# Performance work log

Hardware: AMD Instinct MI355X
Metric: run time of the kernel (lower is better)

The kernel has to match this reference:

```python
import jax, jax.numpy as jnp
import numpy as np

N_PROJECT = 100000
N_COMPANY = 50000
N_EDGES = 1000000
INPUT_DIM = 256
HIDDEN_DIM = 128
NUM_LAYERS = 2
EPS = 1e-12


def setup_inputs() -> dict:
    key = jax.random.key(0)
    ks = jax.random.split(key, 10)
    return {
        "x_project": jax.random.normal(ks[0], (N_PROJECT, INPUT_DIM), jnp.float32),
        "x_company": jax.random.normal(ks[1], (N_COMPANY, INPUT_DIM), jnp.float32),
        "W_project": jax.random.normal(ks[2], (INPUT_DIM, HIDDEN_DIM), jnp.float32) * 0.05,
        "b_project": jax.random.normal(ks[3], (HIDDEN_DIM,), jnp.float32) * 0.05,
        "W_company": jax.random.normal(ks[4], (INPUT_DIM, HIDDEN_DIM), jnp.float32) * 0.05,
        "b_company": jax.random.normal(ks[5], (HIDDEN_DIM,), jnp.float32) * 0.05,
        "pc_src": jax.random.randint(ks[6], (N_EDGES,), 0, N_PROJECT, jnp.int32),
        "pc_dst": jax.random.randint(ks[7], (N_EDGES,), 0, N_COMPANY, jnp.int32),
        "cp_src": jax.random.randint(ks[8], (N_EDGES,), 0, N_COMPANY, jnp.int32),
        "cp_dst": jax.random.randint(ks[9], (N_EDGES,), 0, N_PROJECT, jnp.int32),
    }


def _rel_aggregate(x_src, row, col, num_src, num_dst):
    # D_src^-1/2 A D_dst^-1/2 normalized gather-scale-scatter_add for one relation.
    ones = jnp.ones(row.shape[0], jnp.float32)
    deg_s = jax.ops.segment_sum(ones, row, num_segments=num_src)
    deg_d = jax.ops.segment_sum(ones, col, num_segments=num_dst)
    inv_s = jnp.where(deg_s > 0, deg_s ** -0.5, 0.0)
    inv_d = jnp.where(deg_d > 0, deg_d ** -0.5, 0.0)
    w = inv_s[row] * inv_d[col]                      # [E]
    msg = x_src[row] * w[:, None]                    # [E, H]
    return jax.ops.segment_sum(msg, col, num_segments=num_dst)  # [num_dst, H]


def reference(x_project, x_company, W_project, b_project, W_company, b_company,
              pc_src, pc_dst, cp_src, cp_dst):
    h_p = x_project @ W_project + b_project          # [Np, H]
    h_c = x_company @ W_company + b_company          # [Nc, H]
    acc_p, acc_c = h_p, h_c
    for _ in range(NUM_LAYERS):
        new_p = _rel_aggregate(h_c, cp_src, cp_dst, N_COMPANY, N_PROJECT)
        new_c = _rel_aggregate(h_p, pc_src, pc_dst, N_PROJECT, N_COMPANY)
        h_p, h_c = new_p, new_c
        acc_p = acc_p + h_p
        acc_c = acc_c + h_c
    scale = 1.0 / (NUM_LAYERS + 1)
    out_p = acc_p * scale
    out_c = acc_c * scale
    # F.normalize(p=2, dim=-1)
    out_p = out_p / jnp.maximum(jnp.linalg.norm(out_p, axis=-1, keepdims=True), EPS)
    out_c = out_c / jnp.maximum(jnp.linalg.norm(out_c, axis=-1, keepdims=True), EPS)
    return out_p, out_c
```

## Files before the change

kernel.cpp:

```cpp
#include <hip/hip_runtime.h>
#include <hip/hip_bf16.h>
#include <math.h>

#define HD 128
#define KD 256
#define CAP 64
#define CAPA 96
#define BA 128

typedef __attribute__((ext_vector_type(8))) short bf16x8;
typedef __attribute__((ext_vector_type(4))) float f32x4;

__device__ __forceinline__ unsigned short bfbits(float x) {
    __hip_bfloat16 h = __float2bfloat16(x);
    return *(unsigned short*)&h;
}
__device__ __forceinline__ unsigned int pack_bf2(float a, float b) {
    __hip_bfloat162 h;
    h.x = __float2bfloat16(a);
    h.y = __float2bfloat16(b);
    return *(unsigned int*)&h;
}
__device__ __forceinline__ float2 unpack_bf2(unsigned int u) {
    __hip_bfloat162 h = *(__hip_bfloat162*)&u;
    return __bfloat1622float2(h);
}
__device__ __forceinline__ bf16x8 cvt8(float4 a, float4 b) {
    bf16x8 r;
    r[0] = (short)bfbits(a.x); r[1] = (short)bfbits(a.y);
    r[2] = (short)bfbits(a.z); r[3] = (short)bfbits(a.w);
    r[4] = (short)bfbits(b.x); r[5] = (short)bfbits(b.y);
    r[6] = (short)bfbits(b.z); r[7] = (short)bfbits(b.w);
    return r;
}

__launch_bounds__(256)
__global__ void phaseA(
        const int* __restrict__ cps, const int* __restrict__ cpd,
        int* __restrict__ db0, int* __restrict__ sb0, int* cntD0, int* cntS0,
        const int* __restrict__ pcs, const int* __restrict__ pcd,
        int* __restrict__ db1, int* __restrict__ sb1, int* cntD1, int* cntS1,
        int E, int G0, int G1,
        const float* __restrict__ WA, unsigned short* __restrict__ WtA,
        const float* __restrict__ WB, unsigned short* __restrict__ WtB) {
    __shared__ int curD[512], curS[512];
    const int b = blockIdx.x;
    if (b >= 2 * BA) {
        int idx = (b - 2 * BA) * 256 + threadIdx.x;
        const float* W = (idx < KD * HD) ? WA : WB;
        unsigned short* Wt = (idx < KD * HD) ? WtA : WtB;
        int id = idx & (KD * HD - 1);
        int j = id & 7, lane = (id >> 3) & 63, nt = (id >> 9) & 7, kc = id >> 12;
        int k = kc * 32 + (lane >> 4) * 8 + j;
        int c = nt * 16 + (lane & 15);
        Wt[id] = bfbits(W[k * HD + c]);
        return;
    }
    const int rel = b >> 7;
    const int ib  = b & (BA - 1);
    const int* src = rel ? pcs : cps;
    const int* dst = rel ? pcd : cpd;
    int* db   = rel ? db1 : db0;
    int* sb   = rel ? sb1 : sb0;
    int* cntD = rel ? cntD1 : cntD0;
    int* cntS = rel ? cntS1 : cntS0;
    const int GD  = rel ? G1 : G0;
    const int GS  = rel ? G0 : G1;

    for (int i = threadIdx.x; i < 512; i += 256) { curD[i] = 0; curS[i] = 0; }
    __syncthreads();

    const int chunk = (E + BA - 1) / BA;
    const int e0 = ib * chunk;
    const int e1 = (e0 + chunk < E) ? e0 + chunk : E;
    for (int e = e0 + (int)threadIdx.x; e < e1; e += 256) {
        const int s = src[e];
        const int d = dst[e];
        const int gd = d >> 8;
        const int pd = atomicAdd(&curD[gd], 1);
        if (pd < CAPA)
            db[((size_t)(ib * GD + gd)) * CAPA + pd] = ((d & 255) << 17) | s;
        const int gs = s >> 8;
        const int ps = atomicAdd(&curS[gs], 1);
        if (ps < CAPA)
            sb[((size_t)(ib * GS + gs)) * CAPA + ps] = s;
    }
    __syncthreads();
    for (int g = threadIdx.x; g < GD; g += 256)
        cntD[ib * GD + g] = (curD[g] < CAPA) ? curD[g] : CAPA;
    for (int g = threadIdx.x; g < GS; g += 256)
        cntS[ib * GS + g] = (curS[g] < CAPA) ? curS[g] : CAPA;
}

__launch_bounds__(256, 3)
__global__ void gemm_mfma(const float* __restrict__ X, const unsigned short* __restrict__ Wt,
                          const float* __restrict__ bias,
                          unsigned short* __restrict__ out0, int M) {
    __shared__ __align__(16) char smem[34816];
    uint4* lds4 = (uint4*)smem;
    const unsigned short* lsh = (const unsigned short*)smem;
    float (*eps)[16][132] = (float (*)[16][132])smem;

    const int t = threadIdx.x;
    const int lane = t & 63;
    const int w = t >> 6;
    const int lr = lane & 15;
    const int kb = lane >> 4;
    const int rbase = blockIdx.x * 128;

    f32x4 acc[2][8];
    #pragma unroll
    for (int nt = 0; nt < 8; ++nt) {
        float bv = bias[nt * 16 + lr];
        acc[0][nt] = (f32x4){bv, bv, bv, bv};
        acc[1][nt] = (f32x4){bv, bv, bv, bv};
    }

    const float4* X4 = (const float4*)X;
    const uint4* Wg4 = (const uint4*)Wt;
    const int r0 = rbase + w * 32 + lr;
    const int r1 = r0 + 16;
    const size_t rr0 = (size_t)((r0 < M) ? r0 : 0) * 64 + kb * 2;
    const size_t rr1 = (size_t)((r1 < M) ? r1 : 0) * 64 + kb * 2;

    float4 xf[2][4];
    #pragma unroll
    for (int s = 0; s < 2; ++s) {
        xf[s][0] = X4[rr0 + s * 8];
        xf[s][1] = X4[rr0 + s * 8 + 1];
        xf[s][2] = X4[rr1 + s * 8];
        xf[s][3] = X4[rr1 + s * 8 + 1];
    }

    #pragma unroll
    for (int i = 0; i < 8; ++i) { int q = t + i * 256; lds4[q] = Wg4[q]; }
    __syncthreads();

    #pragma unroll
    for (int kc = 0; kc < 8; ++kc) {
        if (kc == 4) {
            __syncthreads();
            #pragma unroll
            for (int i = 0; i < 8; ++i) { int q = t + i * 256; lds4[q] = Wg4[2048 + q]; }
            __syncthreads();
        }
        const int s = kc & 1;
        bf16x8 a0 = cvt8(xf[s][0], xf[s][1]);
        bf16x8 a1 = cvt8(xf[s][2], xf[s][3]);
        if (kc < 6) {
            xf[s][0] = X4[rr0 + (kc + 2) * 8];
            xf[s][1] = X4[rr0 + (kc + 2) * 8 + 1];
            xf[s][2] = X4[rr1 + (kc + 2) * 8];
            xf[s][3] = X4[rr1 + (kc + 2) * 8 + 1];
        }
        const int slot = kc & 3;
        #pragma unroll
        for (int nt = 0; nt < 8; ++nt) {
            bf16x8 b = *(const bf16x8*)&lsh[(((slot * 8 + nt) * 64) + lane) * 8];
            acc[0][nt] = __builtin_amdgcn_mfma_f32_16x16x32_bf16(a0, b, acc[0][nt], 0, 0, 0);
            acc[1][nt] = __builtin_amdgcn_mfma_f32_16x16x32_bf16(a1, b, acc[1][nt], 0, 0, 0);
        }
    }
    __syncthreads();

    const int er = lane >> 2;
    const int ec = lane & 3;
    #pragma unroll
    for (int mt = 0; mt < 2; ++mt) {
        #pragma unroll
        for (int nt = 0; nt < 8; ++nt)
            #pragma unroll
            for (int reg = 0; reg < 4; ++reg)
                eps[w][kb * 4 + reg][nt * 16 + lr] = acc[mt][nt][reg];
        __syncthreads();
        const int g = rbase + w * 32 + mt * 16 + er;
        if (g < M) {
            #pragma unroll
            for (int i = 0; i < 8; ++i) {
                const int f4c = ec + i * 4;
                float4 v = *(const float4*)&eps[w][er][f4c * 4];
                uint2 u;
                u.x = pack_bf2(v.x, v.y);
                u.y = pack_bf2(v.z, v.w);
                *(uint2*)(out0 + (size_t)g * HD + f4c * 4) = u;
            }
        }
        __syncthreads();
    }
}

__launch_bounds__(256)
__global__ void csrbuild(
        const int* __restrict__ db0, const int* cntD0, int* csr0, int* degs0,
        const int* __restrict__ db1, const int* cntD1, int* csr1, int* degs1,
        const int* __restrict__ sb0, const int* cntS0, int* hist0,
        const int* __restrict__ sb1, const int* cntS1, int* hist1,
        int G0, int G1, int Np, int Nc) {
    __shared__ int rows[256 * 64];
    const int r = blockIdx.x;
    int g, GD, M; const int *bkt, *cnt; int *outp, *degs; bool isCSR;
    if (r < G0) {
        g = r; GD = G0; M = Np; bkt = db0; cnt = cntD0;
        outp = csr0; degs = degs0; isCSR = true;
    } else if (r < G0 + G1) {
        g = r - G0; GD = G1; M = Nc; bkt = db1; cnt = cntD1;
        outp = csr1; degs = degs1; isCSR = true;
    } else if (r < G0 + 2 * G1) {
        g = r - G0 - G1; GD = G1; M = Nc; bkt = sb0; cnt = cntS0;
        outp = hist0; degs = hist0; isCSR = false;
    } else {
        g = r - G0 - 2 * G1; GD = G0; M = Np; bkt = sb1; cnt = cntS1;
        outp = hist1; degs = hist1; isCSR = false;
    }
    const int base = g << 8;
    const int rowsN = ((M - base) < 256) ? (M - base) : 256;
    const int total = BA * CAPA;

    if (isCSR) {
        for (int i = threadIdx.x; i < 256; i += 256) rows[(i << 6) + 63] = 0;
        __syncthreads();
        for (int idx = threadIdx.x; idx < total; idx += 256) {
            const int bb = idx / CAPA;
            const int i  = idx - bb * CAPA;
            if (i < cnt[bb * GD + g]) {
                const unsigned int v =
                    (unsigned int)bkt[((size_t)(bb * GD + g)) * CAPA + i];
                const int dloc = (int)(v >> 17);
                const int s = (int)(v & 0x1FFFF);
                const int p = atomicAdd(&rows[(dloc << 6) + 63], 1);
                if (p < 63) rows[(dloc << 6) + p] = s;
            }
        }
        __syncthreads();
        uint4* dst4 = (uint4*)(outp + ((size_t)base << 6));
        const uint4* src4 = (const uint4*)rows;
        for (int q = threadIdx.x; q < rowsN * 16; q += 256) dst4[q] = src4[q];
        for (int i = threadIdx.x; i < rowsN; i += 256) {
            const int c = rows[(i << 6) + 63];
            degs[base + i] = (c < 63) ? c : 63;
        }
    } else {
        for (int i = threadIdx.x; i < 256; i += 256) rows[i] = 0;
        __syncthreads();
        for (int idx = threadIdx.x; idx < total; idx += 256) {
            const int bb = idx / CAPA;
            const int i  = idx - bb * CAPA;
            if (i < cnt[bb * GD + g]) {
                const int s = bkt[((size_t)(bb * GD + g)) * CAPA + i];
                atomicAdd(&rows[s - base], 1);
            }
        }
        __syncthreads();
        for (int i = threadIdx.x; i < rowsN; i += 256) degs[base + i] = rows[i];
    }
}

__device__ __forceinline__ void agg_gather(const int* __restrict__ degs,
                                           const int* __restrict__ ssrc,
                                           const int* __restrict__ scnt,
                                           const unsigned short* __restrict__ hsrc,
                                           int row, int lane, int q, int cl,
                                           float4& accA, float4& accB) {
    const int deg = degs[row];
    accA = make_float4(0.f, 0.f, 0.f, 0.f);
    accB = make_float4(0.f, 0.f, 0.f, 0.f);
    if (deg > 0) {
        const float id = rsqrtf((float)deg);
        const int n = (deg < CAP) ? deg : CAP;
        int sl = 0; float wl = 0.f;
        if (lane < n) {
            sl = ssrc[((size_t)row << 6) + lane];
            wl = rsqrtf((float)scnt[sl]);
        }
        for (int jj = 0; jj < n; jj += 4) {
            const int j = jj + q;
            const int s = __shfl(sl, j);
            const float wt = __shfl(wl, j) * id;
            const uint4 u = *(const uint4*)(hsrc + (size_t)s * HD + cl * 8);
            const float2 f0 = unpack_bf2(u.x);
            const float2 f1 = unpack_bf2(u.y);
            const float2 f2 = unpack_bf2(u.z);
            const float2 f3 = unpack_bf2(u.w);
            accA.x = fmaf(f0.x, wt, accA.x);
            accA.y = fmaf(f0.y, wt, accA.y);
            accA.z = fmaf(f1.x, wt, accA.z);
            accA.w = fmaf(f1.y, wt, accA.w);
            accB.x = fmaf(f2.x, wt, accB.x);
            accB.y = fmaf(f2.y, wt, accB.y);
            accB.z = fmaf(f3.x, wt, accB.z);
            accB.w = fmaf(f3.y, wt, accB.w);
        }
    }
    accA.x += __shfl_xor(accA.x, 16); accA.y += __shfl_xor(accA.y, 16);
    accA.z += __shfl_xor(accA.z, 16); accA.w += __shfl_xor(accA.w, 16);
    accB.x += __shfl_xor(accB.x, 16); accB.y += __shfl_xor(accB.y, 16);
    accB.z += __shfl_xor(accB.z, 16); accB.w += __shfl_xor(accB.w, 16);
    accA.x += __shfl_xor(accA.x, 32); accA.y += __shfl_xor(accA.y, 32);
    accA.z += __shfl_xor(accA.z, 32); accA.w += __shfl_xor(accA.w, 32);
    accB.x += __shfl_xor(accB.x, 32); accB.y += __shfl_xor(accB.y, 32);
    accB.z += __shfl_xor(accB.z, 32); accB.w += __shfl_xor(accB.w, 32);
}

__global__ void agg_dual(const int* degsA, const int* ssrcA, const int* scntA,
                         const unsigned short* hsrcA, unsigned short* hdstA, int MA,
                         const int* degsB, const int* ssrcB, const int* scntB,
                         const unsigned short* hsrcB, unsigned short* hdstB, int MB) {
    const int bA = (MA + 3) / 4;
    const int lane = threadIdx.x & 63;
    const int q  = lane >> 4;
    const int cl = lane & 15;
    int row;
    const int *degs, *ssrc, *scnt;
    const unsigned short* hsrc; unsigned short* hdst; int M;
    if ((int)blockIdx.x < bA) {
        row = blockIdx.x * 4 + (threadIdx.x >> 6);
        degs = degsA; ssrc = ssrcA; scnt = scntA; hsrc = hsrcA; hdst = hdstA; M = MA;
    } else {
        row = (blockIdx.x - bA) * 4 + (threadIdx.x >> 6);
        degs = degsB; ssrc = ssrcB; scnt = scntB; hsrc = hsrcB; hdst = hdstB; M = MB;
    }
    if (row >= M) return;
    float4 accA, accB;
    agg_gather(degs, ssrc, scnt, hsrc, row, lane, q, cl, accA, accB);
    if (q == 0) {
        uint4 u;
        u.x = pack_bf2(accA.x, accA.y);
        u.y = pack_bf2(accA.z, accA.w);
        u.z = pack_bf2(accB.x, accB.y);
        u.w = pack_bf2(accB.z, accB.w);
        *(uint4*)(hdst + (size_t)row * HD + cl * 8) = u;
    }
}

__global__ void agg_norm_dual(const int* degsA, const int* ssrcA, const int* scntA,
                              const unsigned short* hsrcA, const unsigned short* h0A,
                              const unsigned short* h1A, float* outA, int MA,
                              const int* degsB, const int* ssrcB, const int* scntB,
                              const unsigned short* hsrcB, const unsigned short* h0B,
                              const unsigned short* h1B, float* outB, int MB) {
    const int bA = (MA + 3) / 4;
    const int lane = threadIdx.x & 63;
    const int q  = lane >> 4;
    const int cl = lane & 15;
    int row;
    const int *degs, *ssrc, *scnt;
    const unsigned short *hsrc, *h0, *h1; float* outp; int M;
    if ((int)blockIdx.x < bA) {
        row = blockIdx.x * 4 + (threadIdx.x >> 6);
        degs = degsA; ssrc = ssrcA; scnt = scntA; hsrc = hsrcA;
        h0 = h0A; h1 = h1A; outp = outA; M = MA;
    } else {
        row = (blockIdx.x - bA) * 4 + (threadIdx.x >> 6);
        degs = degsB; ssrc = ssrcB; scnt = scntB; hsrc = hsrcB;
        h0 = h0B; h1 = h1B; outp = outB; M = MB;
    }
    if (row >= M) return;
    float4 accA, accB;
    agg_gather(degs, ssrc, scnt, hsrc, row, lane, q, cl, accA, accB);

    float2 h2;
    if (q == 0)      h2 = make_float2(accA.x, accA.y);
    else if (q == 1) h2 = make_float2(accA.z, accA.w);
    else if (q == 2) h2 = make_float2(accB.x, accB.y);
    else             h2 = make_float2(accB.z, accB.w);

    const int c = cl * 8 + q * 2;
    const size_t base = (size_t)row * HD + c;
    float2 h0v = unpack_bf2(*(const unsigned int*)(h0 + base));
    float2 h1v = unpack_bf2(*(const unsigned int*)(h1 + base));
    const float sc = 1.0f / 3.0f;
    float vx = (h0v.x + h1v.x + h2.x) * sc;
    float vy = (h0v.y + h1v.y + h2.y) * sc;
    float ss = vx * vx + vy * vy;
    #pragma unroll
    for (int off = 1; off < 64; off <<= 1) ss += __shfl_xor(ss, off);
    float inv = 1.0f / fmaxf(sqrtf(ss), 1e-12f);
    *(float2*)(outp + base) = make_float2(vx * inv, vy * inv);
}

extern "C" void kernel_launch(void* const* d_in, const int* in_sizes, int n_in,
                              void* d_out, int out_size, void* d_ws, size_t ws_size,
                              hipStream_t stream) {
    const float* x_p = (const float*)d_in[0];
    const float* x_c = (const float*)d_in[1];
    const float* W_p = (const float*)d_in[2];
    const float* b_p = (const float*)d_in[3];
    const float* W_c = (const float*)d_in[4];
    const float* b_c = (const float*)d_in[5];
    const int* pcs = (const int*)d_in[6];
    const int* pcd = (const int*)d_in[7];
    const int* cps = (const int*)d_in[8];
    const int* cpd = (const int*)d_in[9];

    const int Np = in_sizes[0] / KD;
    const int Nc = in_sizes[1] / KD;
    const int E  = in_sizes[6];

    const int G0 = (Np + 255) >> 8;
    const int G1 = (Nc + 255) >> 8;

    int* scp = (int*)d_ws;
    int* spc = scp + ((size_t)Np << 6);
    int* c_cps = spc + ((size_t)Nc << 6);
    int* c_pcs = c_cps + Nc;
    int* c_cpd = c_pcs + Np;
    int* c_pcd = c_cpd + Np;
    unsigned short* bufP0 = (unsigned short*)(c_pcd + Nc);
    unsigned short* bufC0 = bufP0 + (size_t)Np * HD;
    unsigned short* WtP = bufC0 + (size_t)Nc * HD;
    unsigned short* WtC = WtP + KD * HD;
    int* db0 = (int*)(WtC + KD * HD);
    int* db1 = db0 + (size_t)BA * G0 * CAPA;
    int* sb0 = db1 + (size_t)BA * G1 * CAPA;
    int* sb1 = sb0 + (size_t)BA * G1 * CAPA;
    int* cntD0 = sb1 + (size_t)BA * G0 * CAPA;
    int* cntD1 = cntD0 + BA * G0;
    int* cntS0 = cntD1 + BA * G1;
    int* cntS1 = cntS0 + BA * G1;
    unsigned short* bufP1 = (unsigned short*)db0;
    unsigned short* bufC1 = bufP1 + (size_t)Np * HD;

    float* outP = (float*)d_out;
    float* outC = outP + (size_t)Np * HD;

    const int GP = (Np + 127) / 128;
    const int GC = (Nc + 127) / 128;

    phaseA<<<2 * BA + 256, 256, 0, stream>>>(
        cps, cpd, db0, sb0, cntD0, cntS0,
        pcs, pcd, db1, sb1, cntD1, cntS1,
        E, G0, G1, W_p, WtP, W_c, WtC);

    gemm_mfma<<<GP, 256, 0, stream>>>(x_p, WtP, b_p, bufP0, Np);
    gemm_mfma<<<GC, 256, 0, stream>>>(x_c, WtC, b_c, bufC0, Nc);

    csrbuild<<<2 * (G0 + G1), 256, 0, stream>>>(
        db0, cntD0, scp, c_cpd,
        db1, cntD1, spc, c_pcd,
        sb0, cntS0, c_cps,
        sb1, cntS1, c_pcs,
        G0, G1, Np, Nc);

    const int bP = (Np + 3) / 4, bC = (Nc + 3) / 4;

    agg_dual<<<bP + bC, 256, 0, stream>>>(
        c_cpd, scp, c_cps, bufC0, bufP1, Np,
        c_pcd, spc, c_pcs, bufP0, bufC1, Nc);

    agg_norm_dual<<<bP + bC, 256, 0, stream>>>(
        c_cpd, scp, c_cps, bufC1, bufP0, bufP1, outP, Np,
        c_pcd, spc, c_pcs, bufP1, bufC0, bufC1, outC, Nc);
}
```

Before: 368.9 us.

## Fuse both GEMMs and CSR build into one launch with half-group CSR blocks

Merges the two projection GEMM launches and the CSR/degree-histogram build into a single kernel that dispatches on block index, so independent work can overlap and two launch gaps disappear. CSR build blocks now each handle 128 rows of a 256-row group, which doubles block count and halves shared memory per block so it fits the GEMM's 34816-byte LDS budget and allows higher occupancy. In exchange, every half-block rescans the whole bucket list and discards entries belonging to the other half, doubling the bucket reads.

After: 369.0 us. No clear change (+0.0%).

```diff
diff --git a/kernel.cpp b/kernel.cpp
--- a/kernel.cpp
+++ b/kernel.cpp
@@ -92,11 +92,10 @@
         cntS[ib * GS + g] = (curS[g] < CAPA) ? curS[g] : CAPA;
 }
 
-__launch_bounds__(256, 3)
-__global__ void gemm_mfma(const float* __restrict__ X, const unsigned short* __restrict__ Wt,
-                          const float* __restrict__ bias,
-                          unsigned short* __restrict__ out0, int M) {
-    __shared__ __align__(16) char smem[34816];
+__device__ __forceinline__ void gemm_body(
+        char* smem, const float* __restrict__ X, const unsigned short* __restrict__ Wt,
+        const float* __restrict__ bias, unsigned short* __restrict__ out0,
+        int M, int tile) {
     uint4* lds4 = (uint4*)smem;
     const unsigned short* lsh = (const unsigned short*)smem;
     float (*eps)[16][132] = (float (*)[16][132])smem;
@@ -106,7 +105,7 @@
     const int w = t >> 6;
     const int lr = lane & 15;
     const int kb = lane >> 4;
-    const int rbase = blockIdx.x * 128;
+    const int rbase = tile * 128;
 
     f32x4 acc[2][8];
     #pragma unroll
@@ -189,35 +188,51 @@
     }
 }
 
-__launch_bounds__(256)
-__global__ void csrbuild(
+__launch_bounds__(256, 3)
+__global__ void phaseB(
         const int* __restrict__ db0, const int* cntD0, int* csr0, int* degs0,
         const int* __restrict__ db1, const int* cntD1, int* csr1, int* degs1,
         const int* __restrict__ sb0, const int* cntS0, int* hist0,
         const int* __restrict__ sb1, const int* cntS1, int* hist1,
-        int G0, int G1, int Np, int Nc) {
-    __shared__ int rows[256 * 64];
-    const int r = blockIdx.x;
-    int g, GD, M; const int *bkt, *cnt; int *outp, *degs; bool isCSR;
-    if (r < G0) {
-        g = r; GD = G0; M = Np; bkt = db0; cnt = cntD0;
+        int G0, int G1, int Np, int Nc,
+        const float* Xp, const unsigned short* WtP, const float* bp,
+        unsigned short* h0p, int GP,
+        const float* Xc, const unsigned short* WtC, const float* bc,
+        unsigned short* h0c, int GC) {
+    __shared__ __align__(16) char smem[34816];
+    const int b = blockIdx.x;
+    const int nG = GP + GC;
+    if (b < nG) {
+        if (b < GP) gemm_body(smem, Xp, WtP, bp, h0p, Np, b);
+        else        gemm_body(smem, Xc, WtC, bc, h0c, Nc, b - GP);
+        return;
+    }
+    int r = b - nG;
+    int g, half, GD, M; const int *bkt, *cnt; int *outp, *degs; bool isCSR;
+    if (r < 2 * G0) {
+        g = r >> 1; half = r & 1; GD = G0; M = Np; bkt = db0; cnt = cntD0;
         outp = csr0; degs = degs0; isCSR = true;
-    } else if (r < G0 + G1) {
-        g = r - G0; GD = G1; M = Nc; bkt = db1; cnt = cntD1;
+    } else if (r < 2 * (G0 + G1)) {
+        r -= 2 * G0;
+        g = r >> 1; half = r & 1; GD = G1; M = Nc; bkt = db1; cnt = cntD1;
         outp = csr1; degs = degs1; isCSR = true;
-    } else if (r < G0 + 2 * G1) {
-        g = r - G0 - G1; GD = G1; M = Nc; bkt = sb0; cnt = cntS0;
+    } else if (r < 2 * G0 + 4 * G1) {
+        r -= 2 * (G0 + G1);
+        g = r >> 1; half = r & 1; GD = G1; M = Nc; bkt = sb0; cnt = cntS0;
         outp = hist0; degs = hist0; isCSR = false;
     } else {
-        g = r - G0 - 2 * G1; GD = G0; M = Np; bkt = sb1; cnt = cntS1;
+        r -= 2 * G0 + 4 * G1;
+        g = r >> 1; half = r & 1; GD = G0; M = Np; bkt = sb1; cnt = cntS1;
         outp = hist1; degs = hist1; isCSR = false;
     }
-    const int base = g << 8;
-    const int rowsN = ((M - base) < 256) ? (M - base) : 256;
+    const int base = (g << 8) + (half << 7);
+    const int rowsN = ((M - base) < 128) ? (M - base) : 128;
+    if (rowsN <= 0) return;
+    int* rows = (int*)smem;
     const int total = BA * CAPA;
 
     if (isCSR) {
-        for (int i = threadIdx.x; i < 256; i += 256) rows[(i << 6) + 63] = 0;
+        for (int i = threadIdx.x; i < 128; i += 256) rows[(i << 6) + 63] = 0;
         __syncthreads();
         for (int idx = threadIdx.x; idx < total; idx += 256) {
             const int bb = idx / CAPA;
@@ -226,9 +241,11 @@
                 const unsigned int v =
                     (unsigned int)bkt[((size_t)(bb * GD + g)) * CAPA + i];
                 const int dloc = (int)(v >> 17);
-                const int s = (int)(v & 0x1FFFF);
-                const int p = atomicAdd(&rows[(dloc << 6) + 63], 1);
-                if (p < 63) rows[(dloc << 6) + p] = s;
+                if ((dloc >> 7) == half) {
+                    const int s = (int)(v & 0x1FFFF);
+                    const int p = atomicAdd(&rows[((dloc & 127) << 6) + 63], 1);
+                    if (p < 63) rows[((dloc & 127) << 6) + p] = s;
+                }
             }
         }
         __syncthreads();
@@ -240,14 +257,14 @@
             degs[base + i] = (c < 63) ? c : 63;
         }
     } else {
-        for (int i = threadIdx.x; i < 256; i += 256) rows[i] = 0;
+        for (int i = threadIdx.x; i < 128; i += 256) rows[i] = 0;
         __syncthreads();
         for (int idx = threadIdx.x; idx < total; idx += 256) {
             const int bb = idx / CAPA;
             const int i  = idx - bb * CAPA;
             if (i < cnt[bb * GD + g]) {
-                const int s = bkt[((size_t)(bb * GD + g)) * CAPA + i];
-                atomicAdd(&rows[s - base], 1);
+                const int sloc = bkt[((size_t)(bb * GD + g)) * CAPA + i] - (g << 8);
+                if ((sloc >> 7) == half) atomicAdd(&rows[sloc & 127], 1);
             }
         }
         __syncthreads();
@@ -431,15 +448,14 @@
         pcs, pcd, db1, sb1, cntD1, cntS1,
         E, G0, G1, W_p, WtP, W_c, WtC);
 
-    gemm_mfma<<<GP, 256, 0, stream>>>(x_p, WtP, b_p, bufP0, Np);
-    gemm_mfma<<<GC, 256, 0, stream>>>(x_c, WtC, b_c, bufC0, Nc);
-
-    csrbuild<<<2 * (G0 + G1), 256, 0, stream>>>(
+    phaseB<<<(GP + GC) + 4 * (G0 + G1), 256, 0, stream>>>(
         db0, cntD0, scp, c_cpd,
         db1, cntD1, spc, c_pcd,
         sb0, cntS0, c_cps,
         sb1, cntS1, c_pcs,
-        G0, G1, Np, Nc);
+        G0, G1, Np, Nc,
+        x_p, WtP, b_p, bufP0, GP,
+        x_c, WtC, b_c, bufC0, GC);
 
     const int bP = (Np + 3) / 4, bC = (Nc + 3) / 4;
 
```
